# Optimization experiments

Hardware: AMD Instinct MI355X
Metric: run time of the kernel (lower is better)

## Reference

```python
import jax, jax.numpy as jnp
import numpy as np

LN_EPS = 1e-5
TEMP = 0.1


def get_descriptor(cls, reg):
    # cls: (B, C, H, W), reg: (B, 14, H, W) -> (B, HW, 6)
    B = cls.shape[0]
    scores = jnp.max(cls, axis=1, keepdims=True)          # (B,1,H,W)
    size = reg[:, 3:6]                                     # (B,3,H,W)
    theta = reg[:, 6:7]                                    # (B,1,H,W)
    ori = jnp.concatenate([jnp.sin(theta), jnp.cos(theta)], axis=1)  # (B,2,H,W)
    desc = jnp.concatenate([size, ori, scores], axis=1)    # (B,6,H,W)
    return desc.reshape(B, 6, -1).transpose(0, 2, 1)       # (B,HW,6)


def encode(x, w1, b1, ln_g, ln_b, w2, b2):
    # Linear(6,emb) -> ReLU -> LayerNorm(emb) -> Linear(emb,emb)
    h = jax.nn.relu(x @ w1 + b1)
    mu = jnp.mean(h, axis=-1, keepdims=True)
    var = jnp.var(h, axis=-1, keepdims=True)
    h = (h - mu) * jax.lax.rsqrt(var + LN_EPS) * ln_g + ln_b
    return h @ w2 + b2


def setup_inputs() -> dict:
    key = jax.random.key(0)
    ks = jax.random.split(key, 8)
    B, H, W = 1, 128, 128
    emb = 128
    return {
        "ego_cls": jax.random.normal(ks[0], (B, 2, H, W), jnp.float32),
        "ego_reg": jax.random.normal(ks[1], (B, 14, H, W), jnp.float32),
        "other_cls": jax.random.normal(ks[2], (B, 2, H, W), jnp.float32),
        "other_reg": jax.random.normal(ks[3], (B, 14, H, W), jnp.float32),
        "w1": jax.random.normal(ks[4], (6, emb), jnp.float32) * (1.0 / np.sqrt(6)),
        "b1": jnp.zeros((emb,), jnp.float32),
        "ln_g": jnp.ones((emb,), jnp.float32),
        "ln_b": jnp.zeros((emb,), jnp.float32),
        "w2": jax.random.normal(ks[5], (emb, emb), jnp.float32) * (1.0 / np.sqrt(emb)),
        "b2": jnp.zeros((emb,), jnp.float32),
    }


def reference(ego_cls, ego_reg, other_cls, other_reg, w1, b1, ln_g, ln_b, w2, b2):
    B, num_classes, H, W = ego_cls.shape
    ego_desc = encode(get_descriptor(ego_cls, ego_reg), w1, b1, ln_g, ln_b, w2, b2)      # (B,HW,E)
    other_desc = encode(get_descriptor(other_cls, other_reg), w1, b1, ln_g, ln_b, w2, b2)  # (B,HW,E)
    # full cross-attention (equivalent to the torch block loop)
    attn = jnp.einsum("bqe,bke->bqk", ego_desc, other_desc) / TEMP
    attn_w = jax.nn.softmax(attn, axis=-1)                 # (B,HW,HW)
    other_cls_flat = other_cls.reshape(B, num_classes, -1).transpose(0, 2, 1)  # (B,HW,2)
    other_reg_flat = other_reg.reshape(B, 14, -1).transpose(0, 2, 1)           # (B,HW,14)
    aligned_cls = jnp.einsum("bqk,bkc->bqc", attn_w, other_cls_flat)
    aligned_reg = jnp.einsum("bqk,bkc->bqc", attn_w, other_reg_flat)
    aligned_other_cls = aligned_cls.transpose(0, 2, 1).reshape(B, num_classes, H, W)
    aligned_other_reg = aligned_reg.transpose(0, 2, 1).reshape(B, 14, H, W)
    return (aligned_other_cls, aligned_other_reg)
```

## Files before the change

### kernel.cpp

```cpp
#include <hip/hip_runtime.h>
#include <math.h>

#define N_PIX 16384
#define EMB 128
#define LN_EPS 1e-5f
#define INV_TEMP 10.0f
#define C2 14.4269504f
#define THR2 14.0f
#define RTHR 8.0f
#define BKT 32
#define NTILES (N_PIX / BKT)

typedef __attribute__((ext_vector_type(8))) short short8v;
typedef __attribute__((ext_vector_type(4))) float f32x4;

__device__ __forceinline__ float fexp2(float x) {
#if __has_builtin(__builtin_amdgcn_exp2f)
    return __builtin_amdgcn_exp2f(x);
#else
    float r; asm("v_exp_f32 %0, %1" : "=v"(r) : "v"(x)); return r;
#endif
}

__device__ __forceinline__ unsigned cvt_pk_bf16(float lo, float hi) {
    unsigned r;
    asm("v_cvt_pk_bf16_f32 %0, %1, %2" : "=v"(r) : "v"(lo), "v"(hi));
    return r;
}

__device__ __forceinline__ void split_bf16(float x, unsigned short& h, unsigned short& l) {
    union { float f; unsigned u; } a; a.f = x;
    h = (unsigned short)(a.u >> 16);
    union { unsigned u; float f; } b; b.u = a.u & 0xFFFF0000u;
    float r = x - b.f;
    union { float f; unsigned u; } c; c.f = r;
    unsigned ru = c.u + 0x7FFFu + ((c.u >> 16) & 1u);
    l = (unsigned short)(ru >> 16);
}

__global__ __launch_bounds__(128) void encode_kernel(
    const float* __restrict__ ego_cls, const float* __restrict__ ego_reg,
    const float* __restrict__ other_cls, const float* __restrict__ other_reg,
    const float* __restrict__ w1, const float* __restrict__ b1,
    const float* __restrict__ ln_g, const float* __restrict__ ln_b,
    const float* __restrict__ w2, const float* __restrict__ b2,
    unsigned short* __restrict__ q_hi, unsigned short* __restrict__ q_lo,
    unsigned short* __restrict__ k_hi, unsigned short* __restrict__ k_lo)
{
    int r = blockIdx.x;
    const float* cls; const float* reg; unsigned short *ohi, *olo; int p;
    if (r < N_PIX) { cls = ego_cls;   reg = ego_reg;   ohi = q_hi; olo = q_lo; p = r; }
    else           { cls = other_cls; reg = other_reg; ohi = k_hi; olo = k_lo; p = r - N_PIX; }

    int j = threadIdx.x;

    float x0 = reg[3*N_PIX + p];
    float x1 = reg[4*N_PIX + p];
    float x2 = reg[5*N_PIX + p];
    float th = reg[6*N_PIX + p];
    float x3 = sinf(th);
    float x4 = cosf(th);
    float x5 = fmaxf(cls[p], cls[N_PIX + p]);

    float h = x0*w1[0*EMB+j] + x1*w1[1*EMB+j] + x2*w1[2*EMB+j]
            + x3*w1[3*EMB+j] + x4*w1[4*EMB+j] + x5*w1[5*EMB+j] + b1[j];
    h = fmaxf(h, 0.f);

    __shared__ float hn[EMB];
    __shared__ float red[4];

    float s = h, s2 = h*h;
    #pragma unroll
    for (int off = 32; off >= 1; off >>= 1) {
        s  += __shfl_xor(s,  off);
        s2 += __shfl_xor(s2, off);
    }
    int wid = j >> 6;
    if ((j & 63) == 0) { red[wid] = s; red[2+wid] = s2; }
    __syncthreads();
    float tot  = red[0] + red[1];
    float tot2 = red[2] + red[3];
    float mu  = tot * (1.f/EMB);
    float var = tot2 * (1.f/EMB) - mu*mu;
    float rstd = rsqrtf(var + LN_EPS);
    float hnj = (h - mu) * rstd * ln_g[j] + ln_b[j];
    hn[j] = hnj;
    __syncthreads();

    float acc = b2[j];
    #pragma unroll 8
    for (int k = 0; k < EMB; ++k)
        acc += hn[k] * w2[k*EMB + j];

    unsigned short hb, lb;
    split_bf16(acc, hb, lb);
    ohi[(size_t)p * EMB + j] = hb;
    olo[(size_t)p * EMB + j] = lb;
}

__device__ __forceinline__ void gl_lds16(const void* g, void* l) {
    __builtin_amdgcn_global_load_lds(
        (const __attribute__((address_space(1))) unsigned int*)(g),
        (__attribute__((address_space(3))) unsigned int*)(l), 16, 0, 0);
}

__global__ __launch_bounds__(512, 4) void attn_kernel(
    const unsigned short* __restrict__ Qhi, const unsigned short* __restrict__ Qlo,
    const unsigned short* __restrict__ Khi, const unsigned short* __restrict__ Klo,
    const float* __restrict__ other_cls, const float* __restrict__ other_reg,
    float* __restrict__ macc, float* __restrict__ mbuf, float* __restrict__ lbuf,
    float* __restrict__ out, int S, int TPS, int XPS, int direct)
{
    __shared__ char Ks[4 * 16384];

    const int tid  = threadIdx.x;
    const int w    = tid >> 6, lane = tid & 63;
    const int lg   = lane >> 4, lk = lane & 15;

    const int b  = blockIdx.x;
    const int s  = (b & 7) / XPS;
    const int qb = (b >> 3) * XPS + (b & 7) % XPS;
    const int qt0 = qb * 128 + w * 16;
    const int t0  = s * TPS;
    const int HTPS = TPS >> 1;

    short8v qbh[4], qbl[4];
    {
        const unsigned short* qh = Qhi + (size_t)(qt0 + lk) * EMB + lg*8;
        const unsigned short* ql = Qlo + (size_t)(qt0 + lk) * EMB + lg*8;
        #pragma unroll
        for (int kk = 0; kk < 4; ++kk) {
            qbh[kk] = *(const short8v*)(qh + kk*32);
            qbl[kk] = *(const short8v*)(ql + kk*32);
        }
    }

    const bool stager = (w < 4);
    int st_row[4], st_scol[4], st_pl[4], st_dst[4];
    #pragma unroll
    for (int i = 0; i < 4; ++i) {
        int ci = (w & 3)*4 + i;
        int cb = (ci & 7) * 64 + lane;
        int row  = cb >> 4;
        int colb = (cb & 15) << 4;
        st_pl[i]  = ci >> 3;
        st_row[i] = row;
        st_scol[i] = colb ^ ((row & 7) << 4);
        st_dst[i] = (ci >> 3) * 8192 + (ci & 7) * 1024;
    }

    int koff[4];
    #pragma unroll
    for (int kk = 0; kk < 4; ++kk)
        koff[kk] = (kk*64 + lg*16) ^ ((lk & 7) << 4);

    const float* vplane = (lk < 2) ? (other_cls + lk * N_PIX)
                                   : (other_reg + (lk - 2) * N_PIX);

    float mn = -INFINITY;
    float mtrack = -INFINITY;
    float lrow = 0.f;
    f32x4 accv = {0.f, 0.f, 0.f, 0.f};

    if (stager) {
        #pragma unroll
        for (int sub = 0; sub < 2; ++sub) {
            int kb0 = (t0 + sub) * BKT;
            #pragma unroll
            for (int i = 0; i < 4; ++i) {
                const unsigned short* src = st_pl[i] ? Klo : Khi;
                const char* g = (const char*)src + (((size_t)(kb0 + st_row[i])) << 8) + st_scol[i];
                gl_lds16(g, Ks + sub * 16384 + st_dst[i]);
            }
        }
    }

    int cur = 0;
    for (int it = 0; it < HTPS; ++it) {
        if (stager) {
            if (it + 1 < HTPS) {
                #pragma unroll
                for (int sub = 0; sub < 2; ++sub) {
                    int kn0 = (t0 + 2*(it+1) + sub) * BKT;
                    char* dstb = Ks + ((cur ^ 1) * 2 + sub) * 16384;
                    #pragma unroll
                    for (int i = 0; i < 4; ++i) {
                        const unsigned short* src = st_pl[i] ? Klo : Khi;
                        const char* g = (const char*)src + (((size_t)(kn0 + st_row[i])) << 8) + st_scol[i];
                        gl_lds16(g, dstb + st_dst[i]);
                    }
                }
                asm volatile("s_waitcnt vmcnt(8)" ::: "memory");
            } else {
                asm volatile("s_waitcnt vmcnt(0)" ::: "memory");
            }
        }
        __builtin_amdgcn_sched_barrier(0);
        __builtin_amdgcn_s_barrier();
        __builtin_amdgcn_sched_barrier(0);

        #pragma unroll
        for (int sub = 0; sub < 2; ++sub) {
            const int kb0 = (t0 + 2*it + sub) * BKT;
            const char* Bh = Ks + (cur * 2 + sub) * 16384;
            const char* Bl = Bh + 8192;
            const int rowb = lk * 256;

            short8v ah0r[4], ah1r[4];
            f32x4 S0 = {0,0,0,0}, S1 = {0,0,0,0};
            #pragma unroll
            for (int kk = 0; kk < 4; ++kk) {
                ah0r[kk] = *(const short8v*)(Bh + rowb + koff[kk]);
                ah1r[kk] = *(const short8v*)(Bh + 4096 + rowb + koff[kk]);
            }
            __builtin_amdgcn_s_setprio(1);
            #pragma unroll
            for (int kk = 0; kk < 4; ++kk) {
                S0 = __builtin_amdgcn_mfma_f32_16x16x32_bf16(ah0r[kk], qbh[kk], S0, 0, 0, 0);
                S1 = __builtin_amdgcn_mfma_f32_16x16x32_bf16(ah1r[kk], qbh[kk], S1, 0, 0, 0);
            }
            __builtin_amdgcn_s_setprio(0);

            float mtl = fmaxf(fmaxf(fmaxf(S0[0], S0[1]), fmaxf(S0[2], S0[3])),
                              fmaxf(fmaxf(S1[0], S1[1]), fmaxf(S1[2], S1[3])));
            float mtl2 = mtl * C2;
            if (__any(mtl2 > mtrack - THR2)) {
                float vt[8];
                #pragma unroll
                for (int e = 0; e < 8; ++e)
                    vt[e] = vplane[kb0 + 16*(e>>2) + lg*4 + (e&3)];

                float sc = 1.f;
                if (__any(mtl2 > mn - RTHR)) {
                    float mt = fmaxf(mtl, __shfl_xor(mtl, 16));
                    mt = fmaxf(mt, __shfl_xor(mt, 32));
                    float mt2 = mt * C2;
                    mtrack = fmaxf(mtrack, mt2);

                    __builtin_amdgcn_s_setprio(1);
                    #pragma unroll
                    for (int kk = 0; kk < 4; ++kk) {
                        short8v al0 = *(const short8v*)(Bl + rowb + koff[kk]);
                        short8v al1 = *(const short8v*)(Bl + 4096 + rowb + koff[kk]);
                        S0 = __builtin_amdgcn_mfma_f32_16x16x32_bf16(ah0r[kk], qbl[kk], S0, 0, 0, 0);
                        S1 = __builtin_amdgcn_mfma_f32_16x16x32_bf16(ah1r[kk], qbl[kk], S1, 0, 0, 0);
                        S0 = __builtin_amdgcn_mfma_f32_16x16x32_bf16(al0, qbh[kk], S0, 0, 0, 0);
                        S1 = __builtin_amdgcn_mfma_f32_16x16x32_bf16(al1, qbh[kk], S1, 0, 0, 0);
                    }
                    __builtin_amdgcn_s_setprio(0);

                    if (__any(mt2 > mn + RTHR)) {
                        float mnn = fmaxf(mn, mt2);
                        sc = fexp2(mn - mnn);
                        mn = mnn;
                        #pragma unroll
                        for (int r = 0; r < 4; ++r)
                            accv[r] *= __shfl(sc, lg*4 + r);
                    }
                }

                float p[8]; float rs = 0.f;
                #pragma unroll
                for (int r = 0; r < 4; ++r) { p[r]   = fexp2(fmaf(S0[r], C2, -mn)); rs += p[r];   }
                #pragma unroll
                for (int r = 0; r < 4; ++r) { p[4+r] = fexp2(fmaf(S1[r], C2, -mn)); rs += p[4+r]; }
                lrow = lrow * sc + rs;

                union { short8v v; unsigned u[4]; } pa, vb;
                #pragma unroll
                for (int d = 0; d < 4; ++d) {
                    pa.u[d] = cvt_pk_bf16(p[2*d],  p[2*d+1]);
                    vb.u[d] = cvt_pk_bf16(vt[2*d], vt[2*d+1]);
                }
                __builtin_amdgcn_s_setprio(1);
                accv = __builtin_amdgcn_mfma_f32_16x16x32_bf16(pa.v, vb.v, accv, 0, 0, 0);
                __builtin_amdgcn_s_setprio(0);
            }
        }

        __builtin_amdgcn_sched_barrier(0);
        __builtin_amdgcn_s_barrier();
        __builtin_amdgcn_sched_barrier(0);
        cur ^= 1;
    }

    lrow += __shfl_xor(lrow, 16);
    lrow += __shfl_xor(lrow, 32);

    if (direct) {
        #pragma unroll
        for (int r = 0; r < 4; ++r) {
            float lqr = __shfl(lrow, lg*4 + r);
            out[(size_t)lk * N_PIX + qt0 + lg*4 + r] = accv[r] / lqr;
        }
    } else {
        #pragma unroll
        for (int r = 0; r < 4; ++r)
            macc[((size_t)(s*16 + lk)) * N_PIX + qt0 + lg*4 + r] = accv[r];
        if (lane < 16) {
            mbuf[(size_t)s * N_PIX + qt0 + lane] = mn;
            lbuf[(size_t)s * N_PIX + qt0 + lane] = lrow;
        }
    }
}

__global__ __launch_bounds__(256) void merge_kernel(
    const float* __restrict__ macc, const float* __restrict__ mbuf,
    const float* __restrict__ lbuf, float* __restrict__ out, int S)
{
    int tid = blockIdx.x * 256 + threadIdx.x;
    int q = tid & (N_PIX - 1);
    int c = tid >> 14;
    float M = -INFINITY;
    for (int s = 0; s < S; ++s) M = fmaxf(M, mbuf[s*N_PIX + q]);
    float L = 0.f, O = 0.f;
    for (int s = 0; s < S; ++s) {
        float e = fexp2(mbuf[s*N_PIX + q] - M);
        L += lbuf[s*N_PIX + q] * e;
        O += macc[((size_t)(s*16 + c)) * N_PIX + q] * e;
    }
    out[tid] = O / L;
}

extern "C" void kernel_launch(void* const* d_in, const int* in_sizes, int n_in,
                              void* d_out, int out_size, void* d_ws, size_t ws_size,
                              hipStream_t stream) {
    const float* ego_cls   = (const float*)d_in[0];
    const float* ego_reg   = (const float*)d_in[1];
    const float* other_cls = (const float*)d_in[2];
    const float* other_reg = (const float*)d_in[3];
    const float* w1   = (const float*)d_in[4];
    const float* b1   = (const float*)d_in[5];
    const float* ln_g = (const float*)d_in[6];
    const float* ln_b = (const float*)d_in[7];
    const float* w2   = (const float*)d_in[8];
    const float* b2   = (const float*)d_in[9];

    unsigned short* qhi = (unsigned short*)d_ws;
    unsigned short* qlo = qhi + (size_t)N_PIX*EMB;
    unsigned short* khi = qlo + (size_t)N_PIX*EMB;
    unsigned short* klo = khi + (size_t)N_PIX*EMB;
    const size_t planes_bytes = (size_t)4 * N_PIX * EMB * 2;

    auto need = [&](int S) { return planes_bytes + (size_t)S * N_PIX * 4 * 18; };
    int S = 1, direct = 1;
    if      (ws_size >= need(8)) { S = 8; direct = 0; }
    else if (ws_size >= need(4)) { S = 4; direct = 0; }
    else if (ws_size >= need(2)) { S = 2; direct = 0; }
    int TPS = NTILES / S;
    int XPS = 8 / S;

    float* macc = (float*)((char*)d_ws + planes_bytes);
    float* mbuf = macc + (size_t)S * 16 * N_PIX;
    float* lbuf = mbuf + (size_t)S * N_PIX;

    encode_kernel<<<2*N_PIX, 128, 0, stream>>>(
        ego_cls, ego_reg, other_cls, other_reg,
        w1, b1, ln_g, ln_b, w2, b2, qhi, qlo, khi, klo);

    attn_kernel<<<128*S, 512, 0, stream>>>(
        qhi, qlo, khi, klo, other_cls, other_reg,
        macc, mbuf, lbuf, (float*)d_out, S, TPS, XPS, direct);

    if (!direct)
        merge_kernel<<<(16*N_PIX)/256, 256, 0, stream>>>(
            macc, mbuf, lbuf, (float*)d_out, S);
}
```

Baseline: 253.3 us.

## Process two 16-query tiles per wave to reuse K fragments across queries

Each wave now handles 32 queries (two 16-row sub-tiles A and B) instead of 16, so each K fragment loaded from LDS feeds four MFMAs instead of two, and the grid is halved. The low-part Q fragments are no longer kept in registers but re-read from global memory in the rare refinement path, and the high K fragments are reloaded there too. This halves the number of workgroups, from 128*S to 64*S, which reduces parallelism and may leave CUs idle. It also adds register pressure from the doubled accumulators and per-tile softmax state.

```diff
diff --git a/kernel.cpp b/kernel.cpp
--- a/kernel.cpp
+++ b/kernel.cpp
@@ -120,18 +120,20 @@
     const int b  = blockIdx.x;
     const int s  = (b & 7) / XPS;
     const int qb = (b >> 3) * XPS + (b & 7) % XPS;
-    const int qt0 = qb * 128 + w * 16;
+    const int qt0 = qb * 256 + w * 32;
     const int t0  = s * TPS;
     const int HTPS = TPS >> 1;
 
-    short8v qbh[4], qbl[4];
+    short8v qbhA[4], qbhB[4];
+    const unsigned short* qloA = Qlo + (size_t)(qt0 + lk) * EMB + lg*8;
+    const unsigned short* qloB = qloA + (size_t)16 * EMB;
     {
-        const unsigned short* qh = Qhi + (size_t)(qt0 + lk) * EMB + lg*8;
-        const unsigned short* ql = Qlo + (size_t)(qt0 + lk) * EMB + lg*8;
+        const unsigned short* qhA = Qhi + (size_t)(qt0 + lk) * EMB + lg*8;
+        const unsigned short* qhB = qhA + (size_t)16 * EMB;
         #pragma unroll
         for (int kk = 0; kk < 4; ++kk) {
-            qbh[kk] = *(const short8v*)(qh + kk*32);
-            qbl[kk] = *(const short8v*)(ql + kk*32);
+            qbhA[kk] = *(const short8v*)(qhA + kk*32);
+            qbhB[kk] = *(const short8v*)(qhB + kk*32);
         }
     }
 
@@ -157,10 +159,11 @@
     const float* vplane = (lk < 2) ? (other_cls + lk * N_PIX)
                                    : (other_reg + (lk - 2) * N_PIX);
 
-    float mn = -INFINITY;
-    float mtrack = -INFINITY;
-    float lrow = 0.f;
-    f32x4 accv = {0.f, 0.f, 0.f, 0.f};
+    float mnA = -INFINITY, mnB = -INFINITY;
+    float mtrackA = -INFINITY, mtrackB = -INFINITY;
+    float lrowA = 0.f, lrowB = 0.f;
+    f32x4 accvA = {0.f, 0.f, 0.f, 0.f};
+    f32x4 accvB = {0.f, 0.f, 0.f, 0.f};
 
     if (stager) {
         #pragma unroll
@@ -206,75 +209,132 @@
             const char* Bl = Bh + 8192;
             const int rowb = lk * 256;
 
-            short8v ah0r[4], ah1r[4];
-            f32x4 S0 = {0,0,0,0}, S1 = {0,0,0,0};
-            #pragma unroll
-            for (int kk = 0; kk < 4; ++kk) {
-                ah0r[kk] = *(const short8v*)(Bh + rowb + koff[kk]);
-                ah1r[kk] = *(const short8v*)(Bh + 4096 + rowb + koff[kk]);
-            }
+            f32x4 S0A = {0,0,0,0}, S1A = {0,0,0,0};
+            f32x4 S0B = {0,0,0,0}, S1B = {0,0,0,0};
             __builtin_amdgcn_s_setprio(1);
             #pragma unroll
             for (int kk = 0; kk < 4; ++kk) {
-                S0 = __builtin_amdgcn_mfma_f32_16x16x32_bf16(ah0r[kk], qbh[kk], S0, 0, 0, 0);
-                S1 = __builtin_amdgcn_mfma_f32_16x16x32_bf16(ah1r[kk], qbh[kk], S1, 0, 0, 0);
+                short8v a0 = *(const short8v*)(Bh + rowb + koff[kk]);
+                short8v a1 = *(const short8v*)(Bh + 4096 + rowb + koff[kk]);
+                S0A = __builtin_amdgcn_mfma_f32_16x16x32_bf16(a0, qbhA[kk], S0A, 0, 0, 0);
+                S1A = __builtin_amdgcn_mfma_f32_16x16x32_bf16(a1, qbhA[kk], S1A, 0, 0, 0);
+                S0B = __builtin_amdgcn_mfma_f32_16x16x32_bf16(a0, qbhB[kk], S0B, 0, 0, 0);
+                S1B = __builtin_amdgcn_mfma_f32_16x16x32_bf16(a1, qbhB[kk], S1B, 0, 0, 0);
             }
             __builtin_amdgcn_s_setprio(0);
 
-            float mtl = fmaxf(fmaxf(fmaxf(S0[0], S0[1]), fmaxf(S0[2], S0[3])),
-                              fmaxf(fmaxf(S1[0], S1[1]), fmaxf(S1[2], S1[3])));
-            float mtl2 = mtl * C2;
-            if (__any(mtl2 > mtrack - THR2)) {
+            float mtlA = fmaxf(fmaxf(fmaxf(S0A[0], S0A[1]), fmaxf(S0A[2], S0A[3])),
+                               fmaxf(fmaxf(S1A[0], S1A[1]), fmaxf(S1A[2], S1A[3])));
+            float mtlB = fmaxf(fmaxf(fmaxf(S0B[0], S0B[1]), fmaxf(S0B[2], S0B[3])),
+                               fmaxf(fmaxf(S1B[0], S1B[1]), fmaxf(S1B[2], S1B[3])));
+            bool takeA = __any(mtlA * C2 > mtrackA - THR2);
+            bool takeB = __any(mtlB * C2 > mtrackB - THR2);
+
+            if (takeA || takeB) {
                 float vt[8];
                 #pragma unroll
                 for (int e = 0; e < 8; ++e)
                     vt[e] = vplane[kb0 + 16*(e>>2) + lg*4 + (e&3)];
-
-                float sc = 1.f;
-                if (__any(mtl2 > mn - RTHR)) {
-                    float mt = fmaxf(mtl, __shfl_xor(mtl, 16));
-                    mt = fmaxf(mt, __shfl_xor(mt, 32));
-                    float mt2 = mt * C2;
-                    mtrack = fmaxf(mtrack, mt2);
-
+                union { short8v v; unsigned u[4]; } vb;
+                #pragma unroll
+                for (int d = 0; d < 4; ++d)
+                    vb.u[d] = cvt_pk_bf16(vt[2*d], vt[2*d+1]);
+
+                if (takeA) {
+                    float scA = 1.f;
+                    if (__any(mtlA * C2 > mnA - RTHR)) {
+                        float mtA = fmaxf(mtlA, __shfl_xor(mtlA, 16));
+                        mtA = fmaxf(mtA, __shfl_xor(mtA, 32));
+                        float mtA2 = mtA * C2;
+                        mtrackA = fmaxf(mtrackA, mtA2);
+
+                        __builtin_amdgcn_s_setprio(1);
+                        #pragma unroll
+                        for (int kk = 0; kk < 4; ++kk) {
+                            short8v ah0 = *(const short8v*)(Bh + rowb + koff[kk]);
+                            short8v ah1 = *(const short8v*)(Bh + 4096 + rowb + koff[kk]);
+                            short8v al0 = *(const short8v*)(Bl + rowb + koff[kk]);
+                            short8v al1 = *(const short8v*)(Bl + 4096 + rowb + koff[kk]);
+                            short8v qlA = *(const short8v*)(qloA + kk*32);
+                            S0A = __builtin_amdgcn_mfma_f32_16x16x32_bf16(ah0, qlA, S0A, 0, 0, 0);
+                            S1A = __builtin_amdgcn_mfma_f32_16x16x32_bf16(ah1, qlA, S1A, 0, 0, 0);
+                            S0A = __builtin_amdgcn_mfma_f32_16x16x32_bf16(al0, qbhA[kk], S0A, 0, 0, 0);
+                            S1A = __builtin_amdgcn_mfma_f32_16x16x32_bf16(al1, qbhA[kk], S1A, 0, 0, 0);
+                        }
+                        __builtin_amdgcn_s_setprio(0);
+
+                        if (__any(mtA2 > mnA + RTHR)) {
+                            float mnn = fmaxf(mnA, mtA2);
+                            scA = fexp2(mnA - mnn);
+                            mnA = mnn;
+                            #pragma unroll
+                            for (int r = 0; r < 4; ++r)
+                                accvA[r] *= __shfl(scA, lg*4 + r);
+                        }
+                    }
+                    float p[8]; float rs = 0.f;
+                    #pragma unroll
+                    for (int r = 0; r < 4; ++r) { p[r]   = fexp2(fmaf(S0A[r], C2, -mnA)); rs += p[r];   }
+                    #pragma unroll
+                    for (int r = 0; r < 4; ++r) { p[4+r] = fexp2(fmaf(S1A[r], C2, -mnA)); rs += p[4+r]; }
+                    lrowA = lrowA * scA + rs;
+
+                    union { short8v v; unsigned u[4]; } pa;
+                    #pragma unroll
+                    for (int d = 0; d < 4; ++d)
+                        pa.u[d] = cvt_pk_bf16(p[2*d], p[2*d+1]);
                     __builtin_amdgcn_s_setprio(1);
-                    #pragma unroll
-                    for (int kk = 0; kk < 4; ++kk) {
-                        short8v al0 = *(const short8v*)(Bl + rowb + koff[kk]);
-                        short8v al1 = *(const short8v*)(Bl + 4096 + rowb + koff[kk]);
-                        S0 = __builtin_amdgcn_mfma_f32_16x16x32_bf16(ah0r[kk], qbl[kk], S0, 0, 0, 0);
-                        S1 = __builtin_amdgcn_mfma_f32_16x16x32_bf16(ah1r[kk], qbl[kk], S1, 0, 0, 0);
-                        S0 = __builtin_amdgcn_mfma_f32_16x16x32_bf16(al0, qbh[kk], S0, 0, 0, 0);
-                        S1 = __builtin_amdgcn_mfma_f32_16x16x32_bf16(al1, qbh[kk], S1, 0, 0, 0);
+                    accvA = __builtin_amdgcn_mfma_f32_16x16x32_bf16(pa.v, vb.v, accvA, 0, 0, 0);
+                    __builtin_amdgcn_s_setprio(0);
+                }
+
+                if (takeB) {
+                    float scB = 1.f;
+                    if (__any(mtlB * C2 > mnB - RTHR)) {
+                        float mtB = fmaxf(mtlB, __shfl_xor(mtlB, 16));
+                        mtB = fmaxf(mtB, __shfl_xor(mtB, 32));
+                        float mtB2 = mtB * C2;
+                        mtrackB = fmaxf(mtrackB, mtB2);
+
+                        __builtin_amdgcn_s_setprio(1);
+                        #pragma unroll
+                        for (int kk = 0; kk < 4; ++kk) {
+                            short8v ah0 = *(const short8v*)(Bh + rowb + koff[kk]);
+                            short8v ah1 = *(const short8v*)(Bh + 4096 + rowb + koff[kk]);
+                            short8v al0 = *(const short8v*)(Bl + rowb + koff[kk]);
+                            short8v al1 = *(const short8v*)(Bl + 4096 + rowb + koff[kk]);
+                            short8v qlB = *(const short8v*)(qloB + kk*32);
+                            S0B = __builtin_amdgcn_mfma_f32_16x16x32_bf16(ah0, qlB, S0B, 0, 0, 0);
+                            S1B = __builtin_amdgcn_mfma_f32_16x16x32_bf16(ah1, qlB, S1B, 0, 0, 0);
+                            S0B = __builtin_amdgcn_mfma_f32_16x16x32_bf16(al0, qbhB[kk], S0B, 0, 0, 0);
+                            S1B = __builtin_amdgcn_mfma_f32_16x16x32_bf16(al1, qbhB[kk], S1B, 0, 0, 0);
+                        }
+                        __builtin_amdgcn_s_setprio(0);
+
+                        if (__any(mtB2 > mnB + RTHR)) {
+                            float mnn = fmaxf(mnB, mtB2);
+                            scB = fexp2(mnB - mnn);
+                            mnB = mnn;
+                            #pragma unroll
+                            for (int r = 0; r < 4; ++r)
+                                accvB[r] *= __shfl(scB, lg*4 + r);
+                        }
                     }
+                    float p[8]; float rs = 0.f;
+                    #pragma unroll
+                    for (int r = 0; r < 4; ++r) { p[r]   = fexp2(fmaf(S0B[r], C2, -mnB)); rs += p[r];   }
+                    #pragma unroll
+                    for (int r = 0; r < 4; ++r) { p[4+r] = fexp2(fmaf(S1B[r], C2, -mnB)); rs += p[4+r]; }
+                    lrowB = lrowB * scB + rs;
+
+                    union { short8v v; unsigned u[4]; } pa;
+                    #pragma unroll
+                    for (int d = 0; d < 4; ++d)
+                        pa.u[d] = cvt_pk_bf16(p[2*d], p[2*d+1]);
+                    __builtin_amdgcn_s_setprio(1);
+                    accvB = __builtin_amdgcn_mfma_f32_16x16x32_bf16(pa.v, vb.v, accvB, 0, 0, 0);
                     __builtin_amdgcn_s_setprio(0);
-
-                    if (__any(mt2 > mn + RTHR)) {
-                        float mnn = fmaxf(mn, mt2);
-                        sc = fexp2(mn - mnn);
-                        mn = mnn;
-                        #pragma unroll
-                        for (int r = 0; r < 4; ++r)
-                            accv[r] *= __shfl(sc, lg*4 + r);
-                    }
                 }
-
-                float p[8]; float rs = 0.f;
-                #pragma unroll
-                for (int r = 0; r < 4; ++r) { p[r]   = fexp2(fmaf(S0[r], C2, -mn)); rs += p[r];   }
-                #pragma unroll
-                for (int r = 0; r < 4; ++r) { p[4+r] = fexp2(fmaf(S1[r], C2, -mn)); rs += p[4+r]; }
-                lrow = lrow * sc + rs;
-
-                union { short8v v; unsigned u[4]; } pa, vb;
-                #pragma unroll
-                for (int d = 0; d < 4; ++d) {
-                    pa.u[d] = cvt_pk_bf16(p[2*d],  p[2*d+1]);
-                    vb.u[d] = cvt_pk_bf16(vt[2*d], vt[2*d+1]);
-                }
-                __builtin_amdgcn_s_setprio(1);
-                accv = __builtin_amdgcn_mfma_f32_16x16x32_bf16(pa.v, vb.v, accv, 0, 0, 0);
-                __builtin_amdgcn_s_setprio(0);
             }
         }
 
@@ -284,22 +344,30 @@
         cur ^= 1;
     }
 
-    lrow += __shfl_xor(lrow, 16);
-    lrow += __shfl_xor(lrow, 32);
+    lrowA += __shfl_xor(lrowA, 16);
+    lrowA += __shfl_xor(lrowA, 32);
+    lrowB += __shfl_xor(lrowB, 16);
+    lrowB += __shfl_xor(lrowB, 32);
 
     if (direct) {
         #pragma unroll
         for (int r = 0; r < 4; ++r) {
-            float lqr = __shfl(lrow, lg*4 + r);
-            out[(size_t)lk * N_PIX + qt0 + lg*4 + r] = accv[r] / lqr;
+            float lqA = __shfl(lrowA, lg*4 + r);
+            float lqB = __shfl(lrowB, lg*4 + r);
+            out[(size_t)lk * N_PIX + qt0 + lg*4 + r]      = accvA[r] / lqA;
+            out[(size_t)lk * N_PIX + qt0 + 16 + lg*4 + r] = accvB[r] / lqB;
         }
     } else {
         #pragma unroll
-        for (int r = 0; r < 4; ++r)
-            macc[((size_t)(s*16 + lk)) * N_PIX + qt0 + lg*4 + r] = accv[r];
+        for (int r = 0; r < 4; ++r) {
+            macc[((size_t)(s*16 + lk)) * N_PIX + qt0 + lg*4 + r]      = accvA[r];
+            macc[((size_t)(s*16 + lk)) * N_PIX + qt0 + 16 + lg*4 + r] = accvB[r];
+        }
         if (lane < 16) {
-            mbuf[(size_t)s * N_PIX + qt0 + lane] = mn;
-            lbuf[(size_t)s * N_PIX + qt0 + lane] = lrow;
+            mbuf[(size_t)s * N_PIX + qt0 + lane] = mnA;
+            lbuf[(size_t)s * N_PIX + qt0 + lane] = lrowA;
+            mbuf[(size_t)s * N_PIX + qt0 + 16 + lane] = mnB;
+            lbuf[(size_t)s * N_PIX + qt0 + 16 + lane] = lrowB;
         }
     }
 }
@@ -358,7 +426,7 @@
         ego_cls, ego_reg, other_cls, other_reg,
         w1, b1, ln_g, ln_b, w2, b2, qhi, qlo, khi, klo);
 
-    attn_kernel<<<128*S, 512, 0, stream>>>(
+    attn_kernel<<<64*S, 512, 0, stream>>>(
         qhi, qlo, khi, klo, other_cls, other_reg,
         macc, mbuf, lbuf, (float*)d_out, S, TPS, XPS, direct);
 
```

New measurement: 298.6 us. 1.18x slower.
